# Performance work log

Measured on AMD Instinct MI355X. Metric: run time of the kernel, lower is better.

Reference implementation:

```python
import jax, jax.numpy as jnp
from jax import lax
import numpy as np

K = 4            # prototypes per class: 3 kmeans centroids + 1 backbone
EPS = 0.1        # sinkhorn entropic regularization
MAX_ITER = 100
THRESH = 0.01
KM_ITERS = 10    # Lloyd iterations (replaces host-side sklearn KMeans)
HW = 28          # the original reshapes pred to 28x28, fixing n = 784


def setup_inputs():
    key = jax.random.key(0)
    k1, k2, k3, k4 = jax.random.split(key, 4)
    b, n, d, c = 32, HW * HW, 1024, 20
    return {
        "query": jax.random.normal(k1, (b, n, d), dtype=jnp.float32),
        "score": jax.random.uniform(k2, (b, n, c), dtype=jnp.float32),
        "label": jax.random.randint(k3, (b, c), 0, 2),
        "gt": jax.random.randint(k4, (b, HW, HW), 0, c + 1),
        "weights": jnp.array([1.0, 1.0, 0.0, -1.0], dtype=jnp.float32),
    }


def _assign(dq, cen, selfm):
    # dq [b,m,d], cen [b,c,j,d], selfm [b,c,m] float mask -> one-hot labels, counts
    x2 = jnp.sum(dq * dq, axis=-1)                                   # [b,m]
    d2 = (x2[:, None, :, None]
          - 2.0 * jnp.einsum('bmd,bcjd->bcmj', dq, cen)
          + jnp.sum(cen * cen, axis=-1)[:, :, None, :])              # [b,c,m,j]
    oh = jax.nn.one_hot(jnp.argmin(d2, axis=-1), cen.shape[2], dtype=dq.dtype) * selfm[..., None]
    return oh, oh.sum(axis=2)


def _sinkhorn(Km, u, v):
    # vectorized over the [b,c] pair grid, per-pair early exit as in the torch loop
    def cond(st):
        it, r, cc, done = st
        return (it < MAX_ITER) & jnp.logical_not(jnp.all(done))

    def body(st):
        it, r, cc, done = st
        r1 = u / jnp.einsum('bcnj,bcj->bcn', Km, cc)
        c1 = v / jnp.einsum('bcnj,bcn->bcj', Km, r1)
        err = jnp.mean(jnp.abs(r1 - r), axis=-1)                     # [b,c]
        r = jnp.where(done[..., None], r, r1)
        cc = jnp.where(done[..., None], cc, c1)
        done = done | (err < THRESH)
        return it + 1, r, cc, done

    st = (jnp.int32(0), jnp.ones_like(u), jnp.ones_like(v),
          jnp.zeros(Km.shape[:2], dtype=bool))
    _, r, cc, _ = lax.while_loop(cond, body, st)
    return r[..., :, None] * cc[..., None, :] * Km                   # [b,c,n,K]


def _forward(query, score, label, gt, weights):
    b, n, d = query.shape
    c = score.shape[2]
    dq, ds = query[:, ::2, :], score[:, ::2, :]                      # stride-2 downsample
    m = dq.shape[1]
    cls_assign = jnp.argmax(ds, axis=-1)                             # [b,m]
    sel = cls_assign[:, None, :] == jnp.arange(c)[None, :, None]     # [b,c,m]
    selfm = sel.astype(query.dtype)
    cnt = selfm.sum(-1)                                              # [b,c]
    valid = (label > 0) & (cnt >= K)

    # ---- masked Lloyd's k-means with k-1 = 3 clusters per (image, class) pair
    order = jnp.argsort((~sel).astype(jnp.int32), axis=-1)           # masked points first
    init_idx = order[..., :K - 1]                                    # [b,c,3]
    cen = dq[jnp.arange(b)[:, None, None], init_idx]                 # [b,c,3,d]

    def km_step(cen, _):
        oh, kcnt = _assign(dq, cen, selfm)
        sums = jnp.einsum('bmd,bcmj->bcjd', dq, oh)
        cen = jnp.where(kcnt[..., None] > 0,
                        sums / jnp.maximum(kcnt, 1.0)[..., None], cen)
        return cen, None

    cen, _ = lax.scan(km_step, cen, None, length=KM_ITERS)
    oh, kcnt = _assign(dq, cen, selfm)                               # final labels

    # ---- sort centroids by mean cluster score (descending)
    sm = ds.mean(axis=-1)                                            # [b,m]
    avg = jnp.where(kcnt > 0,
                    jnp.einsum('bm,bcmj->bcj', sm, oh) / jnp.maximum(kcnt, 1.0),
                    -jnp.inf)
    ordj = jnp.argsort(-avg, axis=-1)                                # [b,c,3]
    cen = jnp.take_along_axis(cen, ordj[..., None], axis=2)

    # ---- backbone prototype = mean over unselected downsampled tokens
    un = 1.0 - selfm
    backbone = jnp.einsum('bmd,bcm->bcd', dq, un) / jnp.maximum(m - cnt, 1.0)[..., None]
    protos = jnp.concatenate([cen, backbone[:, :, None, :]], axis=2)  # [b,c,4,d]

    # ---- OT between query[0] tokens and the 4 prototypes (original uses query[0] always)
    q0 = query[0]
    q0h = q0 / jnp.maximum(jnp.linalg.norm(q0, axis=-1, keepdims=True), 1e-12)
    ph = protos / jnp.maximum(jnp.linalg.norm(protos, axis=-1, keepdims=True), 1e-12)
    sim = jnp.einsum('nd,bcjd->bcnj', q0h, ph)                       # [b,c,n,4]
    Km = lax.stop_gradient(jnp.exp(-(1.0 - sim) / EPS))              # torch.no_grad
    u = jnp.full((b, c, n), 1.0 / n, dtype=query.dtype)
    v = jnp.full((b, c, K), 1.0 / K, dtype=query.dtype)
    T = lax.stop_gradient(_sinkhorn(Km, u, v))                       # [b,c,n,4]

    valid = valid & jnp.logical_not(jnp.any(jnp.isnan(T), axis=(2, 3)))
    pred = jnp.einsum('bcnj,j->bcn', T, weights)                     # [b,c,n]

    # ---- BCE vs gt masks (28x28 -> 28x28 bilinear resize is the identity)
    y = (gt.reshape(b, -1)[:, None, :] == (jnp.arange(c) + 1)[None, :, None]).astype(pred.dtype)
    p = jnp.clip(pred, 0.0, 1.0)
    bce = -(y * jnp.maximum(jnp.log(p), -100.0)
            + (1.0 - y) * jnp.maximum(jnp.log(1.0 - p), -100.0)).mean(axis=-1)  # [b,c]
    bce = jnp.where(valid, bce, 0.0)
    total_n = valid.sum().astype(pred.dtype)
    return bce.sum() / (total_n + 1e-4)


def reference(query, score, label, gt, weights):
    return _forward(query, score, label, gt, weights)
```

## Files before the change

kernel.cpp:

```cpp
#include <hip/hip_runtime.h>
#include <cmath>

#define BB 32
#define NN 784
#define MM 392
#define DD 1024
#define CC 20
#define JJ 3
#define KP 4
#define KM_ITERS 10
#define GMAX 64
#define NCOL (BB * CC * KP)
#define NQ0B 98
#define NTSB (BB * 16)

typedef __attribute__((ext_vector_type(8))) short bf16x8;
typedef __attribute__((ext_vector_type(4))) float f32x4;

__device__ inline unsigned short f2bf(float x) {
  unsigned int u = __float_as_uint(x);
  u += 0x7FFFu + ((u >> 16) & 1u);
  return (unsigned short)(u >> 16);
}
__device__ inline float bf2f(unsigned short h) {
  return __uint_as_float(((unsigned int)h) << 16);
}
__device__ inline void f2bf2(float x, unsigned short& hi, unsigned short& lo) {
  hi = f2bf(x);
  lo = f2bf(x - bf2f(hi));
}
__device__ inline void store_bf4(unsigned short* baseh, unsigned short* basel,
                                 int idx4, float4 v) {
  ushort4 h, l;
  f2bf2(v.x, h.x, l.x); f2bf2(v.y, h.y, l.y);
  f2bf2(v.z, h.z, l.z); f2bf2(v.w, h.w, l.w);
  ((ushort4*)baseh)[idx4] = h;
  ((ushort4*)basel)[idx4] = l;
}

__global__ __launch_bounds__(512) void k_prep(
    const float* __restrict__ score, const float* __restrict__ query,
    const int* __restrict__ label,
    int* __restrict__ cls, float* __restrict__ sm, int* __restrict__ valid,
    float* __restrict__ totalsum,
    unsigned short* __restrict__ q0hh, unsigned short* __restrict__ q0hl,
    float* __restrict__ gred) {
  int blk = blockIdx.x;
  int tid = threadIdx.x, lane = tid & 63, wv = tid >> 6;
  __shared__ int s_cnt[CC];
  __shared__ float sa[8][64];

  if (blk < BB) {
    int b = blk;
    if (tid < CC) s_cnt[tid] = 0;
    __syncthreads();
    if (tid < MM) {
      const float4* s4 = (const float4*)(score + ((size_t)b * NN + 2 * tid) * CC);
      float4 r[5];
      #pragma unroll
      for (int k = 0; k < 5; k++) r[k] = s4[k];
      const float* s = (const float*)r;
      float best = s[0]; int bi = 0; float acc = s[0];
      #pragma unroll
      for (int c = 1; c < CC; c++) { float v = s[c]; acc += v; if (v > best) { best = v; bi = c; } }
      cls[b * MM + tid] = bi;
      sm[b * MM + tid] = acc / (float)CC;
      atomicAdd(&s_cnt[bi], 1);
    }
    __syncthreads();
    if (tid < CC) {
      int cv = s_cnt[tid];
      valid[b * CC + tid] = (label[b * CC + tid] > 0 && cv >= KP) ? 1 : 0;
    }
    if (blk == 0 && tid == 0) { gred[0] = 0.f; gred[1] = 0.f; ((int*)gred)[2] = 0; }
  } else if (blk < BB + NQ0B) {
    int n = (blk - BB) * 8 + wv;
    const float* src = query + (size_t)n * DD;
    float v[16];
    float ss = 0.f;
    #pragma unroll
    for (int j = 0; j < 16; j++) { v[j] = src[lane + 64 * j]; ss += v[j] * v[j]; }
    #pragma unroll
    for (int o = 32; o > 0; o >>= 1) ss += __shfl_xor(ss, o, 64);
    float nrm = fmaxf(sqrtf(ss), 1e-12f);
    #pragma unroll
    for (int j = 0; j < 16; j++) {
      unsigned short hi, lo;
      f2bf2(v[j] / nrm, hi, lo);
      q0hh[(size_t)n * DD + lane + 64 * j] = hi;
      q0hl[(size_t)n * DD + lane + 64 * j] = lo;
    }
  } else {
    int t = blk - BB - NQ0B;
    int b = t >> 4, ch = t & 15;
    const float* qb = query + (size_t)b * NN * DD + ch * 64 + lane;
    float a = 0.f;
    #pragma unroll 7
    for (int r = 0; r < 49; r++) {
      int i = wv * 49 + r;
      a += qb[(size_t)(2 * i) * DD];
    }
    sa[wv][lane] = a;
    __syncthreads();
    if (wv == 0) {
      float s = 0.f;
      #pragma unroll
      for (int w = 0; w < 8; w++) s += sa[w][lane];
      totalsum[(size_t)b * DD + ch * 64 + lane] = s;
    }
  }
}

__global__ __launch_bounds__(512) void k_gram(
    const float* __restrict__ query, const int* __restrict__ cls,
    const int* __restrict__ valid, const float* __restrict__ sm,
    const float* __restrict__ totalsum,
    unsigned short* __restrict__ phh, unsigned short* __restrict__ phl) {
  int bc = blockIdx.x;
  if (!valid[bc]) return;
  int b = bc / CC, c = bc - b * CC;
  int tid = threadIdx.x, lane = tid & 63, wv = tid >> 6;
  const float* qb = query + (size_t)b * NN * DD;
  __shared__ int s_wtot[8];
  __shared__ int s_list[GMAX];
  __shared__ __align__(16) float Xs[GMAX][132];
  __shared__ float Gl[GMAX][65];
  __shared__ float s_w[JJ][GMAX];
  __shared__ int s_rank[JJ];
  __shared__ float s_red2[8];

  int flag = 0;
  if (tid < MM) flag = (cls[b * MM + tid] == c) ? 1 : 0;
  unsigned long long msk = __ballot(flag);
  int wp = __popcll(msk & ((1ull << lane) - 1ull));
  if (lane == 0) s_wtot[wv] = __popcll(msk);
  __syncthreads();
  int off = 0, mtot = 0;
  #pragma unroll
  for (int w = 0; w < 8; w++) { int t = s_wtot[w]; if (w < wv) off += t; mtot += t; }
  int mc = mtot > GMAX ? GMAX : mtot;
  if (flag) { int pos = off + wp; if (pos < GMAX) s_list[pos] = tid; }
  __syncthreads();

  const float* pb[4] = {nullptr, nullptr, nullptr, nullptr};
  float* xd[4] = {nullptr, nullptr, nullptr, nullptr};
  #pragma unroll
  for (int s = 0; s < 4; s++) {
    int e = tid + s * 512;
    if (e < mc * 32) {
      pb[s] = qb + (size_t)(2 * s_list[e >> 5]) * DD + (e & 31) * 4;
      xd[s] = &Xs[e >> 5][(e & 31) * 4];
    }
  }

  int T = (mc + 1) >> 1;
  int ntile = T * (T + 1) / 2;
  int ti_[2], tj_[2];
  float a00[2], a01[2], a10[2], a11[2];
  #pragma unroll
  for (int s = 0; s < 2; s++) {
    ti_[s] = -1; tj_[s] = 0;
    a00[s] = 0.f; a01[s] = 0.f; a10[s] = 0.f; a11[s] = 0.f;
    int p = tid + s * 512;
    if (p < ntile) {
      int i = (int)floorf((sqrtf(8.0f * (float)p + 1.0f) - 1.0f) * 0.5f);
      while ((i + 1) * (i + 2) / 2 <= p) i++;
      while (i * (i + 1) / 2 > p) i--;
      ti_[s] = i; tj_[s] = p - i * (i + 1) / 2;
    }
  }

  float4 cur[4], nxt[4];
  #pragma unroll
  for (int s = 0; s < 4; s++) {
    cur[s] = make_float4(0.f, 0.f, 0.f, 0.f);
    nxt[s] = make_float4(0.f, 0.f, 0.f, 0.f);
    if (pb[s]) cur[s] = *(const float4*)(pb[s]);
  }
  for (int ch = 0; ch < 8; ch++) {
    __syncthreads();
    #pragma unroll
    for (int s = 0; s < 4; s++) if (pb[s]) *(float4*)xd[s] = cur[s];
    if (ch < 7) {
      #pragma unroll
      for (int s = 0; s < 4; s++) if (pb[s]) nxt[s] = *(const float4*)(pb[s] + (ch + 1) * 128);
    }
    __syncthreads();
    #pragma unroll
    for (int s = 0; s < 2; s++) {
      if (ti_[s] >= 0) {
        const float4* xr0 = (const float4*)&Xs[2 * ti_[s]][0];
        const float4* xr1 = (const float4*)&Xs[2 * ti_[s] + 1][0];
        const float4* xc0 = (const float4*)&Xs[2 * tj_[s]][0];
        const float4* xc1 = (const float4*)&Xs[2 * tj_[s] + 1][0];
        float s00 = 0.f, s01 = 0.f, s10 = 0.f, s11 = 0.f;
        #pragma unroll
        for (int kk = 0; kk < 32; kk++) {
          float4 u0 = xr0[kk], u1 = xr1[kk], w0 = xc0[kk], w1 = xc1[kk];
          s00 += u0.x * w0.x + u0.y * w0.y + u0.z * w0.z + u0.w * w0.w;
          s01 += u0.x * w1.x + u0.y * w1.y + u0.z * w1.z + u0.w * w1.w;
          s10 += u1.x * w0.x + u1.y * w0.y + u1.z * w0.z + u1.w * w0.w;
          s11 += u1.x * w1.x + u1.y * w1.y + u1.z * w1.z + u1.w * w1.w;
        }
        a00[s] += s00; a01[s] += s01; a10[s] += s10; a11[s] += s11;
      }
    }
    #pragma unroll
    for (int s = 0; s < 4; s++) cur[s] = nxt[s];
  }

  #pragma unroll
  for (int s = 0; s < 2; s++) {
    if (ti_[s] >= 0) {
      int r0 = 2 * ti_[s], r1 = r0 + 1, c0 = 2 * tj_[s], c1 = c0 + 1;
      if (r0 < mc && c0 < mc) { Gl[r0][c0] = a00[s]; Gl[c0][r0] = a00[s]; }
      if (r0 < mc && c1 < mc) { Gl[r0][c1] = a01[s]; Gl[c1][r0] = a01[s]; }
      if (r1 < mc && c0 < mc) { Gl[r1][c0] = a10[s]; Gl[c0][r1] = a10[s]; }
      if (r1 < mc && c1 < mc) { Gl[r1][c1] = a11[s]; Gl[c1][r1] = a11[s]; }
    }
  }
  __syncthreads();

  if (wv == 0) {
    bool act = lane < mc;
    float smv = act ? sm[b * MM + s_list[lane]] : 0.f;
    s_w[0][lane] = (lane == 0) ? 1.f : 0.f;
    s_w[1][lane] = (lane == 1) ? 1.f : 0.f;
    s_w[2][lane] = (lane == 2) ? 1.f : 0.f;
    int aj = 0, n0 = 0, n1 = 0, n2 = 0;
    for (int it = 0; it <= KM_ITERS; it++) {
      float h0 = 0.f, h1 = 0.f, h2 = 0.f;
      if (act) {
        for (int i = 0; i < mc; i++) {
          float g = Gl[lane][i];
          h0 += s_w[0][i] * g; h1 += s_w[1][i] * g; h2 += s_w[2][i] * g;
        }
      }
      float t0 = s_w[0][lane] * h0, t1 = s_w[1][lane] * h1, t2 = s_w[2][lane] * h2;
      for (int o = 1; o < 64; o <<= 1) {
        t0 += __shfl_xor(t0, o, 64); t1 += __shfl_xor(t1, o, 64); t2 += __shfl_xor(t2, o, 64);
      }
      float e0 = t0 - 2.f * h0, e1 = t1 - 2.f * h1, e2 = t2 - 2.f * h2;
      aj = 0; float bv = e0;
      if (e1 < bv) { bv = e1; aj = 1; }
      if (e2 < bv) { bv = e2; aj = 2; }
      n0 = __popcll(__ballot(act && aj == 0));
      n1 = __popcll(__ballot(act && aj == 1));
      n2 = __popcll(__ballot(act && aj == 2));
      if (it == KM_ITERS) break;
      if (act) {
        if (n0 > 0) s_w[0][lane] = (aj == 0) ? 1.f / (float)n0 : 0.f;
        if (n1 > 0) s_w[1][lane] = (aj == 1) ? 1.f / (float)n1 : 0.f;
        if (n2 > 0) s_w[2][lane] = (aj == 2) ? 1.f / (float)n2 : 0.f;
      }
    }
    float s0 = (act && aj == 0) ? smv : 0.f;
    float s1 = (act && aj == 1) ? smv : 0.f;
    float s2 = (act && aj == 2) ? smv : 0.f;
    for (int o = 1; o < 64; o <<= 1) {
      s0 += __shfl_xor(s0, o, 64); s1 += __shfl_xor(s1, o, 64); s2 += __shfl_xor(s2, o, 64);
    }
    if (lane == 0) {
      float avg[JJ];
      avg[0] = (n0 > 0) ? s0 / (float)n0 : -INFINITY;
      avg[1] = (n1 > 0) ? s1 / (float)n1 : -INFINITY;
      avg[2] = (n2 > 0) ? s2 / (float)n2 : -INFINITY;
      bool used[JJ] = {false, false, false};
      for (int s = 0; s < JJ; s++) {
        int bi = -1; float bv = 0.f;
        for (int j = 0; j < JJ; j++)
          if (!used[j] && (bi < 0 || avg[j] > bv)) { bi = j; bv = avg[j]; }
        used[bi] = true; s_rank[bi] = s;
      }
    }
  }
  __syncthreads();

  float4 a0 = make_float4(0.f, 0.f, 0.f, 0.f), a1 = make_float4(0.f, 0.f, 0.f, 0.f);
  int j = tid >> 7, q = tid & 127;
  if (j < 3) {
    for (int g = 0; g < mc; g++) {
      float w = s_w[j][g];
      if (w != 0.f) {
        const float4* row = (const float4*)(qb + (size_t)(2 * s_list[g]) * DD);
        float4 v0 = row[q], v1 = row[q + 128];
        a0.x += w * v0.x; a0.y += w * v0.y; a0.z += w * v0.z; a0.w += w * v0.w;
        a1.x += w * v1.x; a1.y += w * v1.y; a1.z += w * v1.z; a1.w += w * v1.w;
      }
    }
  } else {
    for (int g = 0; g < mc; g++) {
      const float4* row = (const float4*)(qb + (size_t)(2 * s_list[g]) * DD);
      float4 v0 = row[q], v1 = row[q + 128];
      a0.x += v0.x; a0.y += v0.y; a0.z += v0.z; a0.w += v0.w;
      a1.x += v1.x; a1.y += v1.y; a1.z += v1.z; a1.w += v1.w;
    }
    const float4* tb = (const float4*)(totalsum + (size_t)b * DD);
    float4 t0 = tb[q], t1 = tb[q + 128];
    float denom = fmaxf((float)(MM - mtot), 1.f);
    float inv = 1.f / denom;
    a0.x = (t0.x - a0.x) * inv; a0.y = (t0.y - a0.y) * inv;
    a0.z = (t0.z - a0.z) * inv; a0.w = (t0.w - a0.w) * inv;
    a1.x = (t1.x - a1.x) * inv; a1.y = (t1.y - a1.y) * inv;
    a1.z = (t1.z - a1.z) * inv; a1.w = (t1.w - a1.w) * inv;
  }
  float ssq = a0.x * a0.x + a0.y * a0.y + a0.z * a0.z + a0.w * a0.w
            + a1.x * a1.x + a1.y * a1.y + a1.z * a1.z + a1.w * a1.w;
  #pragma unroll
  for (int o = 1; o < 64; o <<= 1) ssq += __shfl_xor(ssq, o, 64);
  if (lane == 0) s_red2[wv] = ssq;
  __syncthreads();
  float nrm = fmaxf(sqrtf(s_red2[2 * j] + s_red2[2 * j + 1]), 1e-12f);
  int prow = (j < 3) ? s_rank[j] : 3;
  size_t rowoff = ((size_t)bc * KP + prow) * DD;
  float4 o0 = make_float4(a0.x / nrm, a0.y / nrm, a0.z / nrm, a0.w / nrm);
  float4 o1 = make_float4(a1.x / nrm, a1.y / nrm, a1.z / nrm, a1.w / nrm);
  store_bf4(phh + rowoff, phl + rowoff, q, o0);
  store_bf4(phh + rowoff, phl + rowoff, q + 128, o1);
}

__global__ __launch_bounds__(64) void k_gemm(
    const unsigned short* __restrict__ Ah, const unsigned short* __restrict__ Al,
    const unsigned short* __restrict__ Bh, const unsigned short* __restrict__ Bl,
    float* __restrict__ P) {
  int n0 = blockIdx.y * 64;
  int m0 = blockIdx.x * 64;
  int lane = threadIdx.x;
  int kh = lane >> 4;
  int lr = lane & 15;

  const unsigned short* pa_h[4]; const unsigned short* pa_l[4];
  #pragma unroll
  for (int mi = 0; mi < 4; mi++) {
    size_t o = (size_t)(m0 + mi * 16 + lr) * DD + kh * 8;
    pa_h[mi] = Ah + o; pa_l[mi] = Al + o;
  }
  const unsigned short* pb_h[4]; const unsigned short* pb_l[4];
  #pragma unroll
  for (int ni = 0; ni < 4; ni++) {
    int col = n0 + ni * 16 + lr;
    size_t o = (size_t)col * DD + kh * 8;
    pb_h[ni] = Bh + o; pb_l[ni] = Bl + o;
  }

  f32x4 acc[4][4];
  #pragma unroll
  for (int mi = 0; mi < 4; mi++)
    #pragma unroll
    for (int ni = 0; ni < 4; ni++) acc[mi][ni] = (f32x4){0.f, 0.f, 0.f, 0.f};

  for (int k0 = 0; k0 < DD; k0 += 32) {
    bf16x8 ah[4], al[4], bh[4], bl[4];
    #pragma unroll
    for (int i = 0; i < 4; i++) {
      ah[i] = *(const bf16x8*)(pa_h[i] + k0);
      al[i] = *(const bf16x8*)(pa_l[i] + k0);
      bh[i] = *(const bf16x8*)(pb_h[i] + k0);
      bl[i] = *(const bf16x8*)(pb_l[i] + k0);
    }
    #pragma unroll
    for (int mi = 0; mi < 4; mi++)
      #pragma unroll
      for (int ni = 0; ni < 4; ni++) {
        acc[mi][ni] = __builtin_amdgcn_mfma_f32_16x16x32_bf16(ah[mi], bh[ni], acc[mi][ni], 0, 0, 0);
        acc[mi][ni] = __builtin_amdgcn_mfma_f32_16x16x32_bf16(ah[mi], bl[ni], acc[mi][ni], 0, 0, 0);
        acc[mi][ni] = __builtin_amdgcn_mfma_f32_16x16x32_bf16(al[mi], bh[ni], acc[mi][ni], 0, 0, 0);
      }
  }

  #pragma unroll
  for (int ni = 0; ni < 4; ni++) {
    int col = n0 + ni * 16 + lr;
    #pragma unroll
    for (int mi = 0; mi < 4; mi++) {
      int m = m0 + mi * 16 + kh * 4;
      if (m < NN) {
        *(f32x4*)(P + (size_t)col * NN + m) = acc[mi][ni];
      }
    }
  }
}

__global__ __launch_bounds__(256) void k_sink(const float* __restrict__ P,
    const int* __restrict__ valid, const int* __restrict__ gt,
    const float* __restrict__ wts, float* __restrict__ gred, float* __restrict__ out) {
  int bc = blockIdx.x; int b = bc / CC, c = bc - b * CC;
  int tid = threadIdx.x;
  int lane = tid & 63, wv = tid >> 6;
  float bce_out = 0.f; int vld_out = 0;

  if (valid[bc]) {
    __shared__ float ccv[KP];
    __shared__ float wred[4][5];
    __shared__ float s_err;
    __shared__ int s_nan;
    float4 kv[4]; float rr[4];
    #pragma unroll
    for (int s4 = 0; s4 < 4; s4++) {
      int n = tid + 256 * s4;
      kv[s4] = make_float4(0.f, 0.f, 0.f, 0.f); rr[s4] = 1.f;
      if (n < NN) {
        float v[KP];
        #pragma unroll
        for (int q = 0; q < KP; q++)
          v[q] = P[((size_t)(4 * bc + q)) * NN + n];
        float4 o;
        o.x = expf(-(1.0f - v[0]) / 0.1f);
        o.y = expf(-(1.0f - v[1]) / 0.1f);
        o.z = expf(-(1.0f - v[2]) / 0.1f);
        o.w = expf(-(1.0f - v[3]) / 0.1f);
        kv[s4] = o;
      }
    }
    if (tid < KP) ccv[tid] = 1.f;
    if (tid == 0) s_nan = 0;
    __syncthreads();
    const float uu = 1.0f / (float)NN, vv = 1.0f / (float)KP;
    for (int it = 0; it < 100; it++) {
      float c0 = ccv[0], c1 = ccv[1], c2 = ccv[2], c3 = ccv[3];
      float dsum = 0.f, p0 = 0.f, p1 = 0.f, p2 = 0.f, p3 = 0.f;
      #pragma unroll
      for (int s4 = 0; s4 < 4; s4++) {
        int n = tid + 256 * s4;
        if (n < NN) {
          float4 k4 = kv[s4];
          float S = k4.x * c0 + k4.y * c1 + k4.z * c2 + k4.w * c3;
          float r1 = uu / S;
          dsum += fabsf(r1 - rr[s4]);
          rr[s4] = r1;
          p0 += k4.x * r1; p1 += k4.y * r1; p2 += k4.z * r1; p3 += k4.w * r1;
        }
      }
      for (int o = 32; o > 0; o >>= 1) {
        dsum += __shfl_down(dsum, o, 64);
        p0 += __shfl_down(p0, o, 64); p1 += __shfl_down(p1, o, 64);
        p2 += __shfl_down(p2, o, 64); p3 += __shfl_down(p3, o, 64);
      }
      if (lane == 0) { wred[wv][0] = dsum; wred[wv][1] = p0; wred[wv][2] = p1; wred[wv][3] = p2; wred[wv][4] = p3; }
      __syncthreads();
      if (tid == 0) {
        float d = 0.f, q0 = 0.f, q1 = 0.f, q2 = 0.f, q3 = 0.f;
        for (int w = 0; w < 4; w++) { d += wred[w][0]; q0 += wred[w][1]; q1 += wred[w][2]; q2 += wred[w][3]; q3 += wred[w][4]; }
        ccv[0] = vv / q0; ccv[1] = vv / q1; ccv[2] = vv / q2; ccv[3] = vv / q3;
        s_err = d / (float)NN;
      }
      __syncthreads();
      if (s_err < 0.01f) break;
    }
    float w0 = wts[0], w1 = wts[1], w2 = wts[2], w3 = wts[3];
    float cc0 = ccv[0], cc1 = ccv[1], cc2 = ccv[2], cc3 = ccv[3];
    float bsum = 0.f; int nanloc = 0;
    const int* gtb = gt + b * NN;
    #pragma unroll
    for (int s4 = 0; s4 < 4; s4++) {
      int n = tid + 256 * s4;
      if (n < NN) {
        float4 k4 = kv[s4];
        float rv = rr[s4];
        float T0 = rv * cc0 * k4.x, T1 = rv * cc1 * k4.y, T2 = rv * cc2 * k4.z, T3 = rv * cc3 * k4.w;
        if (T0 != T0 || T1 != T1 || T2 != T2 || T3 != T3) nanloc = 1;
        float pred = T0 * w0 + T1 * w1 + T2 * w2 + T3 * w3;
        float pcl = fminf(fmaxf(pred, 0.f), 1.f);
        float t = (gtb[n] == c + 1) ? fmaxf(logf(pcl), -100.f) : fmaxf(logf(1.f - pcl), -100.f);
        bsum += t;
      }
    }
    if (nanloc) s_nan = 1;
    for (int o = 32; o > 0; o >>= 1) bsum += __shfl_down(bsum, o, 64);
    if (lane == 0) wred[wv][0] = bsum;
    __syncthreads();
    if (tid == 0) {
      float tot = wred[0][0] + wred[1][0] + wred[2][0] + wred[3][0];
      if (!s_nan) { bce_out = -(tot / (float)NN); vld_out = 1; }
    }
  }

  if (tid == 0) {
    if (vld_out) { atomicAdd(&gred[0], bce_out); atomicAdd(&gred[1], 1.f); }
    __threadfence();
    int old = atomicAdd((int*)gred + 2, 1);
    if (old == BB * CC - 1) {
      float s = atomicAdd(&gred[0], 0.f);
      float n2 = atomicAdd(&gred[1], 0.f);
      out[0] = s / (n2 + 0.0001f);
    }
  }
}

extern "C" void kernel_launch(void* const* d_in, const int* in_sizes, int n_in,
                              void* d_out, int out_size, void* d_ws, size_t ws_size,
                              hipStream_t stream) {
  (void)in_sizes; (void)n_in; (void)out_size; (void)ws_size;
  const float* query = (const float*)d_in[0];
  const float* score = (const float*)d_in[1];
  const int*   label = (const int*)d_in[2];
  const int*   gt    = (const int*)d_in[3];
  const float* wts   = (const float*)d_in[4];
  float* ws = (float*)d_ws;

  size_t off = 0;
  int* cls = (int*)(ws + off);            off += (size_t)BB * MM;
  float* sm = ws + off;                   off += (size_t)BB * MM;
  int* valid = (int*)(ws + off);          off += (size_t)BB * CC;
  float* totalsum = ws + off;             off += (size_t)BB * DD;
  unsigned short* q0hh = (unsigned short*)(ws + off);  off += (size_t)NN * DD / 2;
  unsigned short* q0hl = (unsigned short*)(ws + off);  off += (size_t)NN * DD / 2;
  unsigned short* phh = (unsigned short*)(ws + off);   off += (size_t)BB * CC * KP * DD / 2;
  unsigned short* phl = (unsigned short*)(ws + off);   off += (size_t)BB * CC * KP * DD / 2;
  float* P = ws + off;                    off += (size_t)NCOL * NN;
  float* gred = ws + off;                 off += 16;

  k_prep<<<BB + NQ0B + NTSB, 512, 0, stream>>>(score, query, label, cls, sm, valid,
                                               totalsum, q0hh, q0hl, gred);
  k_gram<<<BB * CC, 512, 0, stream>>>(query, cls, valid, sm, totalsum, phh, phl);
  dim3 gg((NN + 63) / 64, NCOL / 64);
  k_gemm<<<gg, 64, 0, stream>>>(q0hh, q0hl, phh, phl, P);
  k_sink<<<BB * CC, 256, 0, stream>>>(P, valid, gt, wts, gred, (float*)d_out);
}
```

Before: 269.9 us.

## Map Sinkhorn pairs to single wavefronts and widen Gram register tiles

The Sinkhorn kernel now assigns one (b,c) pair to each 64-lane wavefront instead of a 256-thread block. Each lane keeps 13 points in registers, and the per-iteration reductions use xor shuffles, which removes the shared-memory reductions and both block barriers per iteration. Separately, the Gram kernel moves from 2x2 to 4x4 register tiles per thread, so fewer threads each reuse more LDS loads. The costs are higher register pressure, lower occupancy for the Gram step, and less parallelism per Sinkhorn pair.

```diff
diff --git a/kernel.cpp b/kernel.cpp
--- a/kernel.cpp
+++ b/kernel.cpp
@@ -153,21 +153,16 @@
     }
   }
 
-  int T = (mc + 1) >> 1;
+  int T = (mc + 3) >> 2;
   int ntile = T * (T + 1) / 2;
-  int ti_[2], tj_[2];
-  float a00[2], a01[2], a10[2], a11[2];
-  #pragma unroll
-  for (int s = 0; s < 2; s++) {
-    ti_[s] = -1; tj_[s] = 0;
-    a00[s] = 0.f; a01[s] = 0.f; a10[s] = 0.f; a11[s] = 0.f;
-    int p = tid + s * 512;
-    if (p < ntile) {
-      int i = (int)floorf((sqrtf(8.0f * (float)p + 1.0f) - 1.0f) * 0.5f);
-      while ((i + 1) * (i + 2) / 2 <= p) i++;
-      while (i * (i + 1) / 2 > p) i--;
-      ti_[s] = i; tj_[s] = p - i * (i + 1) / 2;
-    }
+  int ti = -1, tj = 0;
+  float a[4][4] = {};
+  if (tid < ntile) {
+    int p = tid;
+    int i = (int)floorf((sqrtf(8.0f * (float)p + 1.0f) - 1.0f) * 0.5f);
+    while ((i + 1) * (i + 2) / 2 <= p) i++;
+    while (i * (i + 1) / 2 > p) i--;
+    ti = i; tj = p - i * (i + 1) / 2;
   }
 
   float4 cur[4], nxt[4];
@@ -186,37 +181,43 @@
       for (int s = 0; s < 4; s++) if (pb[s]) nxt[s] = *(const float4*)(pb[s] + (ch + 1) * 128);
     }
     __syncthreads();
-    #pragma unroll
-    for (int s = 0; s < 2; s++) {
-      if (ti_[s] >= 0) {
-        const float4* xr0 = (const float4*)&Xs[2 * ti_[s]][0];
-        const float4* xr1 = (const float4*)&Xs[2 * ti_[s] + 1][0];
-        const float4* xc0 = (const float4*)&Xs[2 * tj_[s]][0];
-        const float4* xc1 = (const float4*)&Xs[2 * tj_[s] + 1][0];
-        float s00 = 0.f, s01 = 0.f, s10 = 0.f, s11 = 0.f;
+    if (ti >= 0) {
+      const float4* xr0 = (const float4*)&Xs[4 * ti + 0][0];
+      const float4* xr1 = (const float4*)&Xs[4 * ti + 1][0];
+      const float4* xr2 = (const float4*)&Xs[4 * ti + 2][0];
+      const float4* xr3 = (const float4*)&Xs[4 * ti + 3][0];
+      const float4* xc0 = (const float4*)&Xs[4 * tj + 0][0];
+      const float4* xc1 = (const float4*)&Xs[4 * tj + 1][0];
+      const float4* xc2 = (const float4*)&Xs[4 * tj + 2][0];
+      const float4* xc3 = (const float4*)&Xs[4 * tj + 3][0];
+      #pragma unroll 8
+      for (int kk = 0; kk < 32; kk++) {
+        float4 u[4], w[4];
+        u[0] = xr0[kk]; u[1] = xr1[kk]; u[2] = xr2[kk]; u[3] = xr3[kk];
+        w[0] = xc0[kk]; w[1] = xc1[kk]; w[2] = xc2[kk]; w[3] = xc3[kk];
         #pragma unroll
-        for (int kk = 0; kk < 32; kk++) {
-          float4 u0 = xr0[kk], u1 = xr1[kk], w0 = xc0[kk], w1 = xc1[kk];
-          s00 += u0.x * w0.x + u0.y * w0.y + u0.z * w0.z + u0.w * w0.w;
-          s01 += u0.x * w1.x + u0.y * w1.y + u0.z * w1.z + u0.w * w1.w;
-          s10 += u1.x * w0.x + u1.y * w0.y + u1.z * w0.z + u1.w * w0.w;
-          s11 += u1.x * w1.x + u1.y * w1.y + u1.z * w1.z + u1.w * w1.w;
+        for (int r = 0; r < 4; r++)
+          #pragma unroll
+          for (int cq = 0; cq < 4; cq++)
+            a[r][cq] += u[r].x * w[cq].x + u[r].y * w[cq].y
+                      + u[r].z * w[cq].z + u[r].w * w[cq].w;
+      }
+    }
+    #pragma unroll
+    for (int s = 0; s < 4; s++) cur[s] = nxt[s];
+  }
+
+  if (ti >= 0) {
+    #pragma unroll
+    for (int r = 0; r < 4; r++) {
+      int gr = 4 * ti + r;
+      if (gr < mc) {
+        #pragma unroll
+        for (int cq = 0; cq < 4; cq++) {
+          int gc = 4 * tj + cq;
+          if (gc < mc) { Gl[gr][gc] = a[r][cq]; Gl[gc][gr] = a[r][cq]; }
         }
-        a00[s] += s00; a01[s] += s01; a10[s] += s10; a11[s] += s11;
-      }
-    }
-    #pragma unroll
-    for (int s = 0; s < 4; s++) cur[s] = nxt[s];
-  }
-
-  #pragma unroll
-  for (int s = 0; s < 2; s++) {
-    if (ti_[s] >= 0) {
-      int r0 = 2 * ti_[s], r1 = r0 + 1, c0 = 2 * tj_[s], c1 = c0 + 1;
-      if (r0 < mc && c0 < mc) { Gl[r0][c0] = a00[s]; Gl[c0][r0] = a00[s]; }
-      if (r0 < mc && c1 < mc) { Gl[r0][c1] = a01[s]; Gl[c1][r0] = a01[s]; }
-      if (r1 < mc && c0 < mc) { Gl[r1][c0] = a10[s]; Gl[c0][r1] = a10[s]; }
-      if (r1 < mc && c1 < mc) { Gl[r1][c1] = a11[s]; Gl[c1][r1] = a11[s]; }
+      }
     }
   }
   __syncthreads();
@@ -384,80 +385,61 @@
 __global__ __launch_bounds__(256) void k_sink(const float* __restrict__ P,
     const int* __restrict__ valid, const int* __restrict__ gt,
     const float* __restrict__ wts, float* __restrict__ gred, float* __restrict__ out) {
-  int bc = blockIdx.x; int b = bc / CC, c = bc - b * CC;
-  int tid = threadIdx.x;
-  int lane = tid & 63, wv = tid >> 6;
+  int wv = threadIdx.x >> 6, lane = threadIdx.x & 63;
+  int bc = blockIdx.x * 4 + wv;
+  int b = bc / CC, c = bc - b * CC;
   float bce_out = 0.f; int vld_out = 0;
 
   if (valid[bc]) {
-    __shared__ float ccv[KP];
-    __shared__ float wred[4][5];
-    __shared__ float s_err;
-    __shared__ int s_nan;
-    float4 kv[4]; float rr[4];
-    #pragma unroll
-    for (int s4 = 0; s4 < 4; s4++) {
-      int n = tid + 256 * s4;
-      kv[s4] = make_float4(0.f, 0.f, 0.f, 0.f); rr[s4] = 1.f;
+    float4 kv[13]; float rr[13];
+    #pragma unroll
+    for (int s = 0; s < 13; s++) {
+      int n = lane + 64 * s;
+      kv[s] = make_float4(0.f, 0.f, 0.f, 0.f); rr[s] = 1.f;
       if (n < NN) {
-        float v[KP];
-        #pragma unroll
-        for (int q = 0; q < KP; q++)
-          v[q] = P[((size_t)(4 * bc + q)) * NN + n];
         float4 o;
-        o.x = expf(-(1.0f - v[0]) / 0.1f);
-        o.y = expf(-(1.0f - v[1]) / 0.1f);
-        o.z = expf(-(1.0f - v[2]) / 0.1f);
-        o.w = expf(-(1.0f - v[3]) / 0.1f);
-        kv[s4] = o;
-      }
-    }
-    if (tid < KP) ccv[tid] = 1.f;
-    if (tid == 0) s_nan = 0;
-    __syncthreads();
+        o.x = expf(-(1.0f - P[((size_t)(4 * bc + 0)) * NN + n]) / 0.1f);
+        o.y = expf(-(1.0f - P[((size_t)(4 * bc + 1)) * NN + n]) / 0.1f);
+        o.z = expf(-(1.0f - P[((size_t)(4 * bc + 2)) * NN + n]) / 0.1f);
+        o.w = expf(-(1.0f - P[((size_t)(4 * bc + 3)) * NN + n]) / 0.1f);
+        kv[s] = o;
+      }
+    }
     const float uu = 1.0f / (float)NN, vv = 1.0f / (float)KP;
+    float c0 = 1.f, c1 = 1.f, c2 = 1.f, c3 = 1.f;
     for (int it = 0; it < 100; it++) {
-      float c0 = ccv[0], c1 = ccv[1], c2 = ccv[2], c3 = ccv[3];
       float dsum = 0.f, p0 = 0.f, p1 = 0.f, p2 = 0.f, p3 = 0.f;
       #pragma unroll
-      for (int s4 = 0; s4 < 4; s4++) {
-        int n = tid + 256 * s4;
+      for (int s = 0; s < 13; s++) {
+        int n = lane + 64 * s;
         if (n < NN) {
-          float4 k4 = kv[s4];
+          float4 k4 = kv[s];
           float S = k4.x * c0 + k4.y * c1 + k4.z * c2 + k4.w * c3;
           float r1 = uu / S;
-          dsum += fabsf(r1 - rr[s4]);
-          rr[s4] = r1;
+          dsum += fabsf(r1 - rr[s]);
+          rr[s] = r1;
           p0 += k4.x * r1; p1 += k4.y * r1; p2 += k4.z * r1; p3 += k4.w * r1;
         }
       }
-      for (int o = 32; o > 0; o >>= 1) {
-        dsum += __shfl_down(dsum, o, 64);
-        p0 += __shfl_down(p0, o, 64); p1 += __shfl_down(p1, o, 64);
-        p2 += __shfl_down(p2, o, 64); p3 += __shfl_down(p3, o, 64);
-      }
-      if (lane == 0) { wred[wv][0] = dsum; wred[wv][1] = p0; wred[wv][2] = p1; wred[wv][3] = p2; wred[wv][4] = p3; }
-      __syncthreads();
-      if (tid == 0) {
-        float d = 0.f, q0 = 0.f, q1 = 0.f, q2 = 0.f, q3 = 0.f;
-        for (int w = 0; w < 4; w++) { d += wred[w][0]; q0 += wred[w][1]; q1 += wred[w][2]; q2 += wred[w][3]; q3 += wred[w][4]; }
-        ccv[0] = vv / q0; ccv[1] = vv / q1; ccv[2] = vv / q2; ccv[3] = vv / q3;
-        s_err = d / (float)NN;
-      }
-      __syncthreads();
-      if (s_err < 0.01f) break;
+      #pragma unroll
+      for (int o = 1; o < 64; o <<= 1) {
+        dsum += __shfl_xor(dsum, o, 64);
+        p0 += __shfl_xor(p0, o, 64); p1 += __shfl_xor(p1, o, 64);
+        p2 += __shfl_xor(p2, o, 64); p3 += __shfl_xor(p3, o, 64);
+      }
+      c0 = vv / p0; c1 = vv / p1; c2 = vv / p2; c3 = vv / p3;
+      if (dsum / (float)NN < 0.01f) break;
     }
     float w0 = wts[0], w1 = wts[1], w2 = wts[2], w3 = wts[3];
-    float cc0 = ccv[0], cc1 = ccv[1], cc2 = ccv[2], cc3 = ccv[3];
     float bsum = 0.f; int nanloc = 0;
     const int* gtb = gt + b * NN;
     #pragma unroll
-    for (int s4 = 0; s4 < 4; s4++) {
-      int n = tid + 256 * s4;
+    for (int s = 0; s < 13; s++) {
+      int n = lane + 64 * s;
       if (n < NN) {
-        float4 k4 = kv[s4];
-        float rv = rr[s4];
-        float T0 = rv * cc0 * k4.x, T1 = rv * cc1 * k4.y, T2 = rv * cc2 * k4.z, T3 = rv * cc3 * k4.w;
+        float4 k4 = kv[s];
+        float rv = rr[s];
+        float T0 = rv * c0 * k4.x, T1 = rv * c1 * k4.y, T2 = rv * c2 * k4.z, T3 = rv * c3 * k4.w;
         if (T0 != T0 || T1 != T1 || T2 != T2 || T3 != T3) nanloc = 1;
         float pred = T0 * w0 + T1 * w1 + T2 * w2 + T3 * w3;
         float pcl = fminf(fmaxf(pred, 0.f), 1.f);
@@ -465,17 +447,13 @@
         bsum += t;
       }
     }
-    if (nanloc) s_nan = 1;
-    for (int o = 32; o > 0; o >>= 1) bsum += __shfl_down(bsum, o, 64);
-    if (lane == 0) wred[wv][0] = bsum;
-    __syncthreads();
-    if (tid == 0) {
-      float tot = wred[0][0] + wred[1][0] + wred[2][0] + wred[3][0];
-      if (!s_nan) { bce_out = -(tot / (float)NN); vld_out = 1; }
-    }
-  }
-
-  if (tid == 0) {
+    #pragma unroll
+    for (int o = 1; o < 64; o <<= 1) bsum += __shfl_xor(bsum, o, 64);
+    int nanany = __any(nanloc);
+    if (!nanany) { bce_out = -(bsum / (float)NN); vld_out = 1; }
+  }
+
+  if (lane == 0) {
     if (vld_out) { atomicAdd(&gred[0], bce_out); atomicAdd(&gred[1], 1.f); }
     __threadfence();
     int old = atomicAdd((int*)gred + 2, 1);
@@ -515,5 +493,5 @@
   k_gram<<<BB * CC, 512, 0, stream>>>(query, cls, valid, sm, totalsum, phh, phl);
   dim3 gg((NN + 63) / 64, NCOL / 64);
   k_gemm<<<gg, 64, 0, stream>>>(q0hh, q0hl, phh, phl, P);
-  k_sink<<<BB * CC, 256, 0, stream>>>(P, valid, gt, wts, gred, (float*)d_out);
-}
+  k_sink<<<160, 256, 0, stream>>>(P, valid, gt, wts, gred, (float*)d_out);
+}
```

Measured after the change: 309.8 us. 1.15x slower.
